# Performance work log

Measured on AMD Instinct MI355X. Metric: run time of the kernel, lower is better.

Reference implementation:

```python
import jax, jax.numpy as jnp
import numpy as np


def _gru_dir(x, mask, W, U, b, reverse):
    """Keras GRU (reset_after=True) over time with masking.

    x: [B, S, D] float, mask: [B, S] bool, W: [D, 3U], U: [U, 3U], b: [2, 3U].
    Gate order z, r, h. Masked steps carry the previous state/output.
    reverse=True == Keras go_backwards + re-reversed outputs.
    """
    B, S, D = x.shape
    units = U.shape[0]
    b_in, b_rec = b[0], b[1]

    def step(h, inp):
        xt, mt = inp  # xt: [B, D], mt: [B]
        gx = xt @ W + b_in          # [B, 3U]
        gh = h @ U + b_rec          # [B, 3U]
        xz, xr, xh = jnp.split(gx, 3, axis=-1)
        rz, rr, rh = jnp.split(gh, 3, axis=-1)
        z = jax.nn.sigmoid(xz + rz)
        r = jax.nn.sigmoid(xr + rr)
        hh = jnp.tanh(xh + r * rh)
        hn = z * h + (1.0 - z) * hh
        hn = jnp.where(mt[:, None], hn, h)  # masked step: carry state
        return hn, hn

    xs = jnp.swapaxes(x, 0, 1)      # [S, B, D]
    ms = jnp.swapaxes(mask, 0, 1)   # [S, B]
    h0 = jnp.zeros((B, units), x.dtype)
    _, outs = jax.lax.scan(step, h0, (xs, ms), reverse=reverse)
    return jnp.swapaxes(outs, 0, 1)  # [B, S, U]


def setup_inputs() -> dict:
    key = jax.random.key(0)
    ks = jax.random.split(key, 8)
    B, S, V, U = 64, 512, 32000, 256
    x = jax.random.randint(ks[0], (B, S), 0, V, dtype=jnp.int64)
    s = 0.05
    return {
        "x": x,
        "emb": jax.random.normal(ks[1], (V, U), jnp.float32) * s,
        "Wf": jax.random.normal(ks[2], (U, 3 * U), jnp.float32) * s,
        "Uf": jax.random.normal(ks[3], (U, 3 * U), jnp.float32) * s,
        "bf": jax.random.normal(ks[4], (2, 3 * U), jnp.float32) * s,
        "Wb": jax.random.normal(ks[5], (U, 3 * U), jnp.float32) * s,
        "Ub": jax.random.normal(ks[6], (U, 3 * U), jnp.float32) * s,
        "bb": jax.random.normal(ks[7], (2, 3 * U), jnp.float32) * s,
    }


def reference(x, emb, Wf, Uf, bf, Wb, Ub, bb):
    mask = x != 0                 # Embedding(mask_zero=True)
    e = emb[x]                    # [B, S, U]
    fwd = _gru_dir(e, mask, Wf, Uf, bf, reverse=False)
    bwd = _gru_dir(e, mask, Wb, Ub, bb, reverse=True)
    return fwd + bwd              # Bidirectional(merge_mode='sum')
```

## Files before the change

### kernel.cpp

```cpp
#include <hip/hip_runtime.h>
#include <hip/hip_bf16.h>


typedef short short8 __attribute__((ext_vector_type(8)));
typedef float f32x4 __attribute__((ext_vector_type(4)));

__device__ __forceinline__ unsigned short f2bf(float f) {
  unsigned int u = __float_as_uint(f);
  return (unsigned short)((u + 0x7fffu + ((u >> 16) & 1u)) >> 16);
}
__device__ __forceinline__ float blo(unsigned int u) { return __uint_as_float(u << 16); }
__device__ __forceinline__ float bhi(unsigned int u) { return __uint_as_float(u & 0xffff0000u); }
__device__ __forceinline__ float sigf(float x) {
  return __builtin_amdgcn_rcpf(1.f + __expf(-x));
}
__device__ __forceinline__ float tanhfast(float x) {
  return 1.f - 2.f * __builtin_amdgcn_rcpf(1.f + __expf(2.f * x));
}

__global__ void __launch_bounds__(256) wt_prep_kernel(const float* __restrict__ Wf,
                                                      const float* __restrict__ Wb,
                                                      unsigned short* __restrict__ Wtb) {
  int o = blockIdx.x * 256 + threadIdx.x;
  if (o >= 2 * 768 * 256) return;
  int dir = o / (768 * 256);
  int rem = o % (768 * 256);
  int c = rem / 256, k = rem % 256;
  const float* W = dir ? Wb : Wf;
  Wtb[o] = f2bf(W[(size_t)k * 768 + c]);
}

__global__ void __launch_bounds__(256) u_prep_kernel(const float* __restrict__ Uf,
                                                     const float* __restrict__ Ub,
                                                     unsigned short* __restrict__ Upk) {
  int id = blockIdx.x * 256 + threadIdx.x;
  if (id >= 2 * 8 * 6 * 8 * 64) return;
  int lane = id & 63;
  int kk = (id >> 6) & 7;
  int s = (id >> 9) % 6;
  int w = (id / 3072) & 7;
  int dir = id / 24576;
  const float* U = dir ? Ub : Uf;
  int g = s >> 1, d = s & 1;
  int gcol = g * 256 + w * 32 + d * 16 + (lane & 15);
  int k0 = kk * 32 + (lane >> 4) * 8;
  unsigned short* o = Upk + (size_t)id * 8;
#pragma unroll
  for (int e = 0; e < 8; ++e) o[e] = f2bf(U[(size_t)(k0 + e) * 768 + gcol]);
}

__global__ void __launch_bounds__(256) gx_mfma_kernel(
    const int* __restrict__ x, const float* __restrict__ emb,
    const unsigned short* __restrict__ Wtb,
    const float* __restrict__ bfv, const float* __restrict__ bbv,
    unsigned short* __restrict__ gx3) {
  __shared__ __align__(16) unsigned short As[128 * 32];
  __shared__ __align__(16) unsigned short Bs[128 * 32];
  __shared__ int xid[128];

  int tid = threadIdx.x;
  int r0 = blockIdx.x * 128;
  int yt = blockIdx.y;
  int dir = (yt >= 6) ? 1 : 0;
  int c0 = (yt - dir * 6) * 128;
  const float* bv = dir ? bbv : bfv;
  const unsigned short* WtD = Wtb + (size_t)dir * 768 * 256;

  if (tid < 128) xid[tid] = x[r0 + tid];
  __syncthreads();

  int lane = tid & 63, w = tid >> 6;
  int wr = w >> 1, wc = w & 1;

  f32x4 acc[4][4] = {};

  for (int ks = 0; ks < 8; ++ks) {
#pragma unroll
    for (int i = 0; i < 2; ++i) {
      int s = tid + i * 256;
      int row = s >> 2, kslot = s & 3;
      int sw = kslot ^ ((row >> 2) & 3);
      const float* src = emb + (size_t)xid[row] * 256 + ks * 32 + kslot * 8;
      float4 f0 = *(const float4*)src;
      float4 f1 = *(const float4*)(src + 4);
      uint4 pa;
      pa.x = f2bf(f0.x) | ((unsigned)f2bf(f0.y) << 16);
      pa.y = f2bf(f0.z) | ((unsigned)f2bf(f0.w) << 16);
      pa.z = f2bf(f1.x) | ((unsigned)f2bf(f1.y) << 16);
      pa.w = f2bf(f1.z) | ((unsigned)f2bf(f1.w) << 16);
      *(uint4*)&As[row * 32 + sw * 8] = pa;
      uint4 pb = *(const uint4*)(WtD + (size_t)(c0 + row) * 256 + ks * 32 + kslot * 8);
      *(uint4*)&Bs[row * 32 + sw * 8] = pb;
    }
    __syncthreads();

    short8 a[4], b[4];
#pragma unroll
    for (int f = 0; f < 4; ++f) {
      int rowA = wr * 64 + f * 16 + (lane & 15);
      int swA = (lane >> 4) ^ ((rowA >> 2) & 3);
      a[f] = __builtin_bit_cast(short8, *(const uint4*)&As[rowA * 32 + swA * 8]);
      int rowB = wc * 64 + f * 16 + (lane & 15);
      int swB = (lane >> 4) ^ ((rowB >> 2) & 3);
      b[f] = __builtin_bit_cast(short8, *(const uint4*)&Bs[rowB * 32 + swB * 8]);
    }
#pragma unroll
    for (int fm = 0; fm < 4; ++fm)
#pragma unroll
      for (int fn = 0; fn < 4; ++fn)
        acc[fm][fn] = __builtin_amdgcn_mfma_f32_16x16x32_bf16(a[fm], b[fn], acc[fm][fn], 0, 0, 0);
    __syncthreads();
  }

#pragma unroll
  for (int fn = 0; fn < 4; ++fn) {
    int col = c0 + wc * 64 + fn * 16 + (lane & 15);
    float bias = bv[col] + (col < 512 ? bv[768 + col] : 0.f);
    int g = col >> 8, u = col & 255;
    int w2 = u >> 5, d = (u >> 4) & 1, cl2 = u & 15;
    int s = g * 2 + d;
#pragma unroll
    for (int fm = 0; fm < 4; ++fm) {
      int rowb = r0 + wr * 64 + fm * 16 + (lane >> 4) * 4;
#pragma unroll
      for (int q = 0; q < 4; ++q) {
        int row = rowb + q;
        int bb2 = row >> 9, tt2 = row & 511;
        int G = bb2 & 3, bg2 = bb2 >> 2;
        size_t idx = ((((size_t)(dir * 512 + tt2) * 16 + bg2) * 8 + w2) * 64
                      + (G * 16 + cl2)) * 6 + s;
        gx3[idx] = f2bf(acc[fm][fn][q] + bias);
      }
    }
  }
}

__global__ void __launch_bounds__(512, 1) gru_kernel(
    const unsigned short* __restrict__ Upk,
    const unsigned short* __restrict__ gx3,
    const int* __restrict__ x,
    const float* __restrict__ bfv, const float* __restrict__ bbv,
    float* __restrict__ out) {
  int wg = blockIdx.x;
  int dir = wg >> 4, bg = wg & 15;
  int tid = threadIdx.x;
  int w = tid >> 6, l = tid & 63;
  int G = l >> 4, cl = l & 15;
  int b = bg * 4 + G;

  __shared__ __align__(16) unsigned short h_lds[2][4096];

  short8 Ufr[6][8];
  {
    const unsigned short* ub = Upk + (size_t)(dir * 8 + w) * 24576 + (size_t)l * 8;
#pragma unroll
    for (int s = 0; s < 6; ++s)
#pragma unroll
      for (int kk = 0; kk < 8; ++kk)
        Ufr[s][kk] = __builtin_bit_cast(short8, *(const uint4*)(ub + (s * 8 + kk) * 512));
  }

  {
    uint4 z = {0u, 0u, 0u, 0u};
    ((uint4*)h_lds)[tid] = z;
    ((uint4*)h_lds)[512 + tid] = z;
  }

  const float* bv = dir ? bbv : bfv;
  float brh[2];
#pragma unroll
  for (int d = 0; d < 2; ++d) brh[d] = bv[1280 + w * 32 + d * 16 + cl];
  const int* xb = x + b * 512;
  float* outb = out + ((size_t)b << 17);
  const unsigned short* gxb = gx3 + ((size_t)bg * 8 + w) * 384 + (size_t)l * 6;

  int amask = (cl & 7) << 4;
  float h_old[2] = {0.f, 0.f};

  int t0 = dir ? 511 : 0;
  unsigned int gq0, gq1, gq2;
  int xv;
  {
    const unsigned short* g = gxb + (size_t)(dir * 512 + t0) * 49152;
    gq0 = *(const unsigned int*)(g);
    gq1 = *(const unsigned int*)(g + 2);
    gq2 = *(const unsigned int*)(g + 4);
    xv = xb[t0];
  }
  __syncthreads();

  int cur = 0;
  for (int step = 0; step < 512; ++step) {
    int tcur = dir ? (511 - step) : step;
    int sn = (step < 511) ? step + 1 : 511;
    int tn = dir ? (511 - sn) : sn;
    unsigned int gn0, gn1, gn2;
    int xn;
    {
      const unsigned short* g = gxb + (size_t)(dir * 512 + tn) * 49152;
      gn0 = *(const unsigned int*)(g);
      gn1 = *(const unsigned int*)(g + 2);
      gn2 = *(const unsigned int*)(g + 4);
      xn = xb[tn];
    }

    f32x4 acc[6];
#pragma unroll
    for (int s = 0; s < 6; ++s) acc[s] = (f32x4){0.f, 0.f, 0.f, 0.f};
    const char* hb = (const char*)(&h_lds[cur][0]);
#pragma unroll
    for (int kk = 0; kk < 8; ++kk) {
      short8 a = __builtin_bit_cast(short8,
          *(const uint4*)(hb + cl * 512 + (((kk << 6) | (G << 4)) ^ amask)));
#pragma unroll
      for (int s = 0; s < 6; ++s)
        acc[s] = __builtin_amdgcn_mfma_f32_16x16x32_bf16(a, Ufr[s][kk], acc[s], 0, 0, 0);
    }

    char* hw = (char*)(&h_lds[cur ^ 1][0]);
#pragma unroll
    for (int d = 0; d < 2; ++d) {
      float gz = d ? bhi(gq0) : blo(gq0);
      float gr = d ? bhi(gq1) : blo(gq1);
      float gh = d ? bhi(gq2) : blo(gq2);
      float z = sigf(gz + acc[0 + d][0]);
      float r = sigf(gr + acc[2 + d][0]);
      float hh = tanhfast(gh + r * (acc[4 + d][0] + brh[d]));
      float hn = hh + z * (h_old[d] - hh);
      hn = (xv == 0) ? h_old[d] : hn;
      h_old[d] = hn;
      int u = w * 32 + d * 16 + cl;
      *(unsigned short*)(hw + G * 2048 + ((u * 2) ^ ((G & 1) << 6))) = f2bf(hn);
      atomicAdd(&outb[(size_t)tcur * 256 + u], hn);
    }
    __syncthreads();
    gq0 = gn0; gq1 = gn1; gq2 = gn2; xv = xn;
    cur ^= 1;
  }
}

extern "C" void kernel_launch(void* const* d_in, const int* in_sizes, int n_in,
                              void* d_out, int out_size, void* d_ws, size_t ws_size,
                              hipStream_t stream) {
  const int*   x   = (const int*)d_in[0];
  const float* emb = (const float*)d_in[1];
  const float* Wf  = (const float*)d_in[2];
  const float* Uf  = (const float*)d_in[3];
  const float* bf_ = (const float*)d_in[4];
  const float* Wb  = (const float*)d_in[5];
  const float* Ub  = (const float*)d_in[6];
  const float* bb_ = (const float*)d_in[7];
  float* out = (float*)d_out;

  unsigned short* gx3 = (unsigned short*)d_ws;
  unsigned short* Wtb = (unsigned short*)((char*)d_ws + 100663296);
  unsigned short* Upk = (unsigned short*)((char*)d_ws + 100663296 + 786432);

  hipMemsetAsync(d_out, 0, (size_t)out_size * sizeof(float), stream);

  wt_prep_kernel<<<1536, 256, 0, stream>>>(Wf, Wb, Wtb);
  u_prep_kernel<<<192, 256, 0, stream>>>(Uf, Ub, Upk);
  gx_mfma_kernel<<<dim3(256, 12), 256, 0, stream>>>(x, emb, Wtb, bf_, bb_, gx3);
  gru_kernel<<<32, 512, 0, stream>>>(Upk, gx3, x, bf_, bb_, out);
}
```

Baseline: 691.8 us.

## Split gate-major gx layout, pointer-increment prefetch, and LDS-only step barrier

The precomputed input-gate buffer changes from interleaved 6-value records to a gate-major layout. Each gate plane is then contiguous per step, and a lane's three loads become coalesced 4-byte reads at fixed offsets. The recurrent loop now advances pointers incrementally instead of recomputing indices from the step. It also replaces __syncthreads with a barrier that waits only on LDS counters, so the global prefetch loads stay in flight across the barrier. This relies on the global loads not being needed until the next step, and the sched_barrier calls constrain compiler scheduling.

```diff
diff --git a/kernel.cpp b/kernel.cpp
--- a/kernel.cpp
+++ b/kernel.cpp
@@ -16,6 +16,12 @@
 }
 __device__ __forceinline__ float tanhfast(float x) {
   return 1.f - 2.f * __builtin_amdgcn_rcpf(1.f + __expf(2.f * x));
+}
+__device__ __forceinline__ void lds_barrier() {
+  __builtin_amdgcn_sched_barrier(0);
+  asm volatile("s_waitcnt lgkmcnt(0)" ::: "memory");
+  __builtin_amdgcn_s_barrier();
+  __builtin_amdgcn_sched_barrier(0);
 }
 
 __global__ void __launch_bounds__(256) wt_prep_kernel(const float* __restrict__ Wf,
@@ -53,7 +59,7 @@
     const int* __restrict__ x, const float* __restrict__ emb,
     const unsigned short* __restrict__ Wtb,
     const float* __restrict__ bfv, const float* __restrict__ bbv,
-    unsigned short* __restrict__ gx3) {
+    unsigned short* __restrict__ gx4) {
   __shared__ __align__(16) unsigned short As[128 * 32];
   __shared__ __align__(16) unsigned short Bs[128 * 32];
   __shared__ int xid[128];
@@ -118,7 +124,6 @@
     float bias = bv[col] + (col < 512 ? bv[768 + col] : 0.f);
     int g = col >> 8, u = col & 255;
     int w2 = u >> 5, d = (u >> 4) & 1, cl2 = u & 15;
-    int s = g * 2 + d;
 #pragma unroll
     for (int fm = 0; fm < 4; ++fm) {
       int rowb = r0 + wr * 64 + fm * 16 + (lane >> 4) * 4;
@@ -127,9 +132,9 @@
         int row = rowb + q;
         int bb2 = row >> 9, tt2 = row & 511;
         int G = bb2 & 3, bg2 = bb2 >> 2;
-        size_t idx = ((((size_t)(dir * 512 + tt2) * 16 + bg2) * 8 + w2) * 64
-                      + (G * 16 + cl2)) * 6 + s;
-        gx3[idx] = f2bf(acc[fm][fn][q] + bias);
+        size_t idx = ((size_t)(dir * 512 + tt2) * 3 + g) * 16384
+                     + (size_t)((bg2 * 8 + w2) * 64 + (G * 16 + cl2)) * 2 + d;
+        gx4[idx] = f2bf(acc[fm][fn][q] + bias);
       }
     }
   }
@@ -137,7 +142,7 @@
 
 __global__ void __launch_bounds__(512, 1) gru_kernel(
     const unsigned short* __restrict__ Upk,
-    const unsigned short* __restrict__ gx3,
+    const unsigned short* __restrict__ gx4,
     const int* __restrict__ x,
     const float* __restrict__ bfv, const float* __restrict__ bbv,
     float* __restrict__ out) {
@@ -170,39 +175,33 @@
   float brh[2];
 #pragma unroll
   for (int d = 0; d < 2; ++d) brh[d] = bv[1280 + w * 32 + d * 16 + cl];
-  const int* xb = x + b * 512;
   float* outb = out + ((size_t)b << 17);
-  const unsigned short* gxb = gx3 + ((size_t)bg * 8 + w) * 384 + (size_t)l * 6;
 
   int amask = (cl & 7) << 4;
   float h_old[2] = {0.f, 0.f};
 
   int t0 = dir ? 511 : 0;
-  unsigned int gq0, gq1, gq2;
-  int xv;
-  {
-    const unsigned short* g = gxb + (size_t)(dir * 512 + t0) * 49152;
-    gq0 = *(const unsigned int*)(g);
-    gq1 = *(const unsigned int*)(g + 2);
-    gq2 = *(const unsigned int*)(g + 4);
-    xv = xb[t0];
-  }
+  long sdelta = dir ? -98304 : 98304;
+  const char* gp = (const char*)gx4 + ((size_t)(dir * 512 + t0) * 98304)
+                   + (size_t)((bg * 8 + w) * 64 + l) * 4;
+  const int* xp = x + b * 512 + t0;
+  int xdelta = dir ? -1 : 1;
+
+  unsigned int gq0 = *(const unsigned int*)(gp);
+  unsigned int gq1 = *(const unsigned int*)(gp + 32768);
+  unsigned int gq2 = *(const unsigned int*)(gp + 65536);
+  int xv = *xp;
   __syncthreads();
 
   int cur = 0;
+  int tcur = t0;
   for (int step = 0; step < 512; ++step) {
-    int tcur = dir ? (511 - step) : step;
-    int sn = (step < 511) ? step + 1 : 511;
-    int tn = dir ? (511 - sn) : sn;
-    unsigned int gn0, gn1, gn2;
-    int xn;
-    {
-      const unsigned short* g = gxb + (size_t)(dir * 512 + tn) * 49152;
-      gn0 = *(const unsigned int*)(g);
-      gn1 = *(const unsigned int*)(g + 2);
-      gn2 = *(const unsigned int*)(g + 4);
-      xn = xb[tn];
-    }
+    const char* gpn = (step < 511) ? gp + sdelta : gp;
+    const int* xpn = (step < 511) ? xp + xdelta : xp;
+    unsigned int gn0 = *(const unsigned int*)(gpn);
+    unsigned int gn1 = *(const unsigned int*)(gpn + 32768);
+    unsigned int gn2 = *(const unsigned int*)(gpn + 65536);
+    int xn = *xpn;
 
     f32x4 acc[6];
 #pragma unroll
@@ -233,8 +232,10 @@
       *(unsigned short*)(hw + G * 2048 + ((u * 2) ^ ((G & 1) << 6))) = f2bf(hn);
       atomicAdd(&outb[(size_t)tcur * 256 + u], hn);
     }
-    __syncthreads();
+    lds_barrier();
     gq0 = gn0; gq1 = gn1; gq2 = gn2; xv = xn;
+    gp = gpn; xp = xpn;
+    tcur += (step < 511) ? xdelta : 0;
     cur ^= 1;
   }
 }
@@ -252,7 +253,7 @@
   const float* bb_ = (const float*)d_in[7];
   float* out = (float*)d_out;
 
-  unsigned short* gx3 = (unsigned short*)d_ws;
+  unsigned short* gx4 = (unsigned short*)d_ws;
   unsigned short* Wtb = (unsigned short*)((char*)d_ws + 100663296);
   unsigned short* Upk = (unsigned short*)((char*)d_ws + 100663296 + 786432);
 
@@ -260,6 +261,6 @@
 
   wt_prep_kernel<<<1536, 256, 0, stream>>>(Wf, Wb, Wtb);
   u_prep_kernel<<<192, 256, 0, stream>>>(Uf, Ub, Upk);
-  gx_mfma_kernel<<<dim3(256, 12), 256, 0, stream>>>(x, emb, Wtb, bf_, bb_, gx3);
-  gru_kernel<<<32, 512, 0, stream>>>(Upk, gx3, x, bf_, bb_, out);
-}
+  gx_mfma_kernel<<<dim3(256, 12), 256, 0, stream>>>(x, emb, Wtb, bf_, bb_, gx4);
+  gru_kernel<<<32, 512, 0, stream>>>(Upk, gx4, x, bf_, bb_, out);
+}
```

Result: faster. 607.4 us (median of 2 runs) (-12.2%).
